# Performance work log

Hardware: AMD Instinct MI355X
Metric: run time of the kernel (lower is better)

The kernel has to match this reference:

```python
import jax, jax.numpy as jnp
import numpy as np

B, C, H, W = 2, 64, 512, 896


def setup_inputs() -> dict:
    key = jax.random.key(0)
    k1, k2 = jax.random.split(key)
    feature = jax.random.normal(k1, (B, C, H, W), dtype=jnp.float32)
    # flow in pixel units; a few pixels of motion is typical for video frames
    flow = jax.random.normal(k2, (B, 2, H, W), dtype=jnp.float32) * 3.0
    return {"feature": feature, "flow": flow}


def reference(feature, flow):
    # Flownet2-style Resample2d: out[b,c,y,x] = bilinear(feature[b,c], y+v, x+u)
    # with zero contribution from out-of-bounds taps.
    Bv, Cv, Hv, Wv = feature.shape
    HW = Hv * Wv
    gx = flow[:, 0] + jnp.arange(Wv, dtype=flow.dtype)[None, None, :]  # [B,H,W]
    gy = flow[:, 1] + jnp.arange(Hv, dtype=flow.dtype)[None, :, None]  # [B,H,W]
    x0f = jnp.floor(gx)
    y0f = jnp.floor(gy)
    wx = gx - x0f  # frac weights
    wy = gy - y0f
    x0 = x0f.astype(jnp.int32)
    y0 = y0f.astype(jnp.int32)
    feat = feature.reshape(Bv, Cv, HW)

    def corner(xi, yi, w):
        # zero out-of-bounds taps; clip indices so the gather is always legal
        valid = (xi >= 0) & (xi < Wv) & (yi >= 0) & (yi < Hv)
        idx = jnp.clip(yi, 0, Hv - 1) * Wv + jnp.clip(xi, 0, Wv - 1)  # [B,H,W]
        idx = jnp.broadcast_to(idx.reshape(Bv, 1, HW), (Bv, Cv, HW))
        v = jnp.take_along_axis(feat, idx, axis=2)  # [B,C,HW]
        wm = (w * valid.astype(w.dtype)).reshape(Bv, 1, HW)
        return v * wm

    out = (
        corner(x0, y0, (1.0 - wx) * (1.0 - wy))
        + corner(x0 + 1, y0, wx * (1.0 - wy))
        + corner(x0, y0 + 1, (1.0 - wx) * wy)
        + corner(x0 + 1, y0 + 1, wx * wy)
    )
    return out.reshape(Bv, Cv, Hv, Wv)
```

## Files before the change

kernel.cpp:

```cpp
#include <hip/hip_runtime.h>


#define Bv 2
#define Cv 64
#define Hv 512
#define Wv 896
#define HWsz (Hv * Wv)

#define TILE 64
#define CPB 2
#define NCG (Cv / CPB)
#define SW 91
#define SH 88
#define XOFF 12
#define YOFF 11
#define NSITES (SH * SW)
#define NTX (Wv / TILE)
#define NTY (Hv / TILE)
#define NTILES (NTX * NTY)
#define NBLK (Bv * NCG * NTILES)
#define THREADS 1024
#define NW (THREADS / 64)
#define KITERS (TILE * TILE / THREADS)

__global__ __launch_bounds__(THREADS, 8) void resample2d_kernel(
    const float* __restrict__ feature,
    const float* __restrict__ flow,
    float* __restrict__ out) {
    __shared__ float2 smem[NSITES];

    const int orig = blockIdx.x;
    const int wid = (orig & 7) * (NBLK / 8) + (orig >> 3);
    const int txi = wid % NTX;
    const int t2 = wid / NTX;
    const int tyi = t2 % NTY;
    const int zb = t2 / NTY;
    const int b = zb / NCG;
    const int c0 = (zb % NCG) * CPB;

    const int tx0 = txi * TILE;
    const int ty0 = tyi * TILE;
    const int xs = tx0 - XOFF;
    const int ys = ty0 - YOFF;

    const int tid = threadIdx.x;
    const int lane = tid & 63;
    const int wv = tid >> 6;

    const float* __restrict__ fbase = feature + ((size_t)b * Cv + c0) * HWsz;
    const float* __restrict__ flb = flow + (size_t)b * 2 * HWsz;
    float* __restrict__ ob = out + ((size_t)b * Cv + c0) * HWsz;

    const int px = tx0 + lane;
    float u[KITERS], v[KITERS];
#pragma unroll
    for (int k = 0; k < KITERS; ++k) {
        const int y = ty0 + wv + NW * k;
        const int pix = y * Wv + px;
        u[k] = flb[pix];
        v[k] = flb[HWsz + pix];
    }

    const bool interior = (xs >= 0) & (xs + SW <= Wv) & (ys >= 0) & (ys + SH <= Hv);
    if (interior) {
#pragma unroll
        for (int k = 0; k < 8; ++k) {
            const int p = tid + THREADS * k;
            if (p < NSITES) {
                const int r = p / SW;
                const int xx = p - r * SW;
                const float* src = fbase + (size_t)(ys + r) * Wv + (xs + xx);
                float2 val;
                val.x = src[0];
                val.y = src[HWsz];
                smem[p] = val;
            }
        }
    } else {
#pragma unroll
        for (int k = 0; k < 8; ++k) {
            const int p = tid + THREADS * k;
            if (p < NSITES) {
                const int r = p / SW;
                const int xx = p - r * SW;
                const int gy = ys + r;
                const int gx = xs + xx;
                float2 val = make_float2(0.0f, 0.0f);
                if (((unsigned)gy < (unsigned)Hv) & ((unsigned)gx < (unsigned)Wv)) {
                    const float* src = fbase + (size_t)gy * Wv + gx;
                    val.x = src[0];
                    val.y = src[HWsz];
                }
                smem[p] = val;
            }
        }
    }

    float wx[KITERS], wy[KITERS];
    int ac[KITERS];
    unsigned iw = 0;
#pragma unroll
    for (int k = 0; k < KITERS; ++k) {
        const int y = ty0 + wv + NW * k;
        const float gx = u[k] + (float)px;
        const float gy = v[k] + (float)y;
        const float x0f = floorf(gx);
        const float y0f = floorf(gy);
        wx[k] = gx - x0f;
        wy[k] = gy - y0f;
        const int lx = (int)x0f - xs;
        const int ly = (int)y0f - ys;
        const bool inwin = ((unsigned)lx <= (unsigned)(SW - 2)) &
                           ((unsigned)ly <= (unsigned)(SH - 2));
        iw |= inwin ? (1u << k) : 0u;
        const int lxc = min(max(lx, 0), SW - 2);
        const int lyc = min(max(ly, 0), SH - 2);
        ac[k] = lyc * SW + lxc;
    }

    __syncthreads();

#define READ(T, K)                        \
    do {                                  \
        const int a_ = ac[K];             \
        T[0] = smem[a_];                  \
        T[1] = smem[a_ + 1];              \
        T[2] = smem[a_ + SW];             \
        T[3] = smem[a_ + SW + 1];         \
    } while (0)

#define CONSUME(T, K)                                                          \
    do {                                                                       \
        if (!(iw & (1u << (K)))) {            \
            const int y_ = ty0 + wv + NW * (K);                                \
            const float gx_ = u[K] + (float)px;                                \
            const float gy_ = v[K] + (float)y_;                                \
            const int x0_ = (int)floorf(gx_);                                  \
            const int y0_ = (int)floorf(gy_);                                  \
            const int x1_ = x0_ + 1, y1_ = y0_ + 1;                            \
            const bool vx0 = (unsigned)x0_ < (unsigned)Wv;                     \
            const bool vx1 = (unsigned)x1_ < (unsigned)Wv;                     \
            const bool vy0 = (unsigned)y0_ < (unsigned)Hv;                     \
            const bool vy1 = (unsigned)y1_ < (unsigned)Hv;                     \
            const int cx0 = min(max(x0_, 0), Wv - 1);                          \
            const int cx1 = min(max(x1_, 0), Wv - 1);                          \
            const int cy0 = min(max(y0_, 0), Hv - 1);                          \
            const int cy1 = min(max(y1_, 0), Hv - 1);                          \
            _Pragma("unroll") for (int c = 0; c < CPB; ++c) {                  \
                const float* f = fbase + (size_t)c * HWsz;                     \
                ((float*)&T[0])[c] = (vx0 & vy0) ? f[cy0 * Wv + cx0] : 0.0f;   \
                ((float*)&T[1])[c] = (vx1 & vy0) ? f[cy0 * Wv + cx1] : 0.0f;   \
                ((float*)&T[2])[c] = (vx0 & vy1) ? f[cy1 * Wv + cx0] : 0.0f;   \
                ((float*)&T[3])[c] = (vx1 & vy1) ? f[cy1 * Wv + cx1] : 0.0f;   \
            }                                                                  \
        }                                                                      \
        const float omx = 1.0f - wx[K];                                        \
        const float omy = 1.0f - wy[K];                                        \
        const float w00 = omx * omy;                                           \
        const float w10 = wx[K] * omy;                                         \
        const float w01 = omx * wy[K];                                         \
        const float w11 = wx[K] * wy[K];                                       \
        const int pix_ = (ty0 + wv + NW * (K)) * Wv + px;                      \
        const float r0 = T[0].x * w00 + T[1].x * w10 +                         \
                         T[2].x * w01 + T[3].x * w11;                          \
        const float r1 = T[0].y * w00 + T[1].y * w10 +                         \
                         T[2].y * w01 + T[3].y * w11;                          \
        __builtin_nontemporal_store(r0, &ob[pix_]);                            \
        __builtin_nontemporal_store(r1, &ob[HWsz + pix_]);                     \
    } while (0)

    float2 tA[4], tB[4];
    READ(tA, 0);
    READ(tB, 1);
    CONSUME(tA, 0);
    READ(tA, 2);
    CONSUME(tB, 1);
    READ(tB, 3);
    CONSUME(tA, 2);
    CONSUME(tB, 3);

#undef READ
#undef CONSUME
}

extern "C" void kernel_launch(void* const* d_in, const int* in_sizes, int n_in,
                              void* d_out, int out_size, void* d_ws, size_t ws_size,
                              hipStream_t stream) {
    const float* feature = (const float*)d_in[0];
    const float* flow = (const float*)d_in[1];
    float* out = (float*)d_out;

    dim3 block(THREADS, 1, 1);
    dim3 grid(NBLK, 1, 1);
    resample2d_kernel<<<grid, block, 0, stream>>>(feature, flow, out);
}
```

Baseline: 428.2 us.

## Process four channel pairs per block with double-buffered LDS staging

Each block now handles four channel-pair groups instead of one. Flow, bilinear weights and window addresses are computed once and reused across the groups, and the next group's feature window is loaded into registers while the current group is computed from a double-buffered LDS tile. The aim is to amortise the flow load and per-pixel address math, and to overlap global loads with compute. In exchange LDS use doubles, the launch-bounds occupancy hint drops, grid size shrinks fourfold, and there are more barriers per block.

Result: no change. 425.3 us (-0.7%).

```diff
diff --git a/kernel.cpp b/kernel.cpp
--- a/kernel.cpp
+++ b/kernel.cpp
@@ -9,7 +9,9 @@
 
 #define TILE 64
 #define CPB 2
+#define GPB 4
 #define NCG (Cv / CPB)
+#define NCGB (NCG / GPB)
 #define SW 91
 #define SH 88
 #define XOFF 12
@@ -18,16 +20,20 @@
 #define NTX (Wv / TILE)
 #define NTY (Hv / TILE)
 #define NTILES (NTX * NTY)
-#define NBLK (Bv * NCG * NTILES)
+#define NBLK (Bv * NCGB * NTILES)
 #define THREADS 1024
 #define NW (THREADS / 64)
 #define KITERS (TILE * TILE / THREADS)
-
-__global__ __launch_bounds__(THREADS, 8) void resample2d_kernel(
+#define SITE_ITERS ((NSITES + THREADS - 1) / THREADS)
+#define LDS_BYTES (2 * NSITES * (int)sizeof(float2))
+
+__global__ __launch_bounds__(THREADS, 4) void resample2d_kernel(
     const float* __restrict__ feature,
     const float* __restrict__ flow,
     float* __restrict__ out) {
-    __shared__ float2 smem[NSITES];
+    extern __shared__ float2 smem[];
+    float2* const buf0 = smem;
+    float2* const buf1 = smem + NSITES;
 
     const int orig = blockIdx.x;
     const int wid = (orig & 7) * (NBLK / 8) + (orig >> 3);
@@ -35,8 +41,8 @@
     const int t2 = wid / NTX;
     const int tyi = t2 % NTY;
     const int zb = t2 / NTY;
-    const int b = zb / NCG;
-    const int c0 = (zb % NCG) * CPB;
+    const int b = zb / NCGB;
+    const int c0 = (zb % NCGB) * (GPB * CPB);
 
     const int tx0 = txi * TILE;
     const int ty0 = tyi * TILE;
@@ -53,50 +59,53 @@
 
     const int px = tx0 + lane;
     float u[KITERS], v[KITERS];
+    int pixk[KITERS];
 #pragma unroll
     for (int k = 0; k < KITERS; ++k) {
         const int y = ty0 + wv + NW * k;
-        const int pix = y * Wv + px;
-        u[k] = flb[pix];
-        v[k] = flb[HWsz + pix];
-    }
-
-    const bool interior = (xs >= 0) & (xs + SW <= Wv) & (ys >= 0) & (ys + SH <= Hv);
-    if (interior) {
+        pixk[k] = y * Wv + px;
+        u[k] = flb[pixk[k]];
+        v[k] = flb[HWsz + pixk[k]];
+    }
+
+    int sOff[SITE_ITERS];
+    int gOff[SITE_ITERS];
+    float vmask[SITE_ITERS];
 #pragma unroll
-        for (int k = 0; k < 8; ++k) {
-            const int p = tid + THREADS * k;
-            if (p < NSITES) {
-                const int r = p / SW;
-                const int xx = p - r * SW;
-                const float* src = fbase + (size_t)(ys + r) * Wv + (xs + xx);
-                float2 val;
-                val.x = src[0];
-                val.y = src[HWsz];
-                smem[p] = val;
-            }
-        }
-    } else {
-#pragma unroll
-        for (int k = 0; k < 8; ++k) {
-            const int p = tid + THREADS * k;
-            if (p < NSITES) {
-                const int r = p / SW;
-                const int xx = p - r * SW;
-                const int gy = ys + r;
-                const int gx = xs + xx;
-                float2 val = make_float2(0.0f, 0.0f);
-                if (((unsigned)gy < (unsigned)Hv) & ((unsigned)gx < (unsigned)Wv)) {
-                    const float* src = fbase + (size_t)gy * Wv + gx;
-                    val.x = src[0];
-                    val.y = src[HWsz];
-                }
-                smem[p] = val;
-            }
-        }
-    }
-
-    float wx[KITERS], wy[KITERS];
+    for (int i = 0; i < SITE_ITERS; ++i) {
+        const int p = tid + THREADS * i;
+        const int pc = (p < NSITES) ? p : (NSITES - 1);
+        const int r = pc / SW;
+        const int xx = pc - r * SW;
+        const int gy = ys + r;
+        const int gx = xs + xx;
+        const bool vd = ((unsigned)gy < (unsigned)Hv) & ((unsigned)gx < (unsigned)Wv);
+        gOff[i] = vd ? (gy * Wv + gx) : 0;
+        vmask[i] = vd ? 1.0f : 0.0f;
+        sOff[i] = pc;
+    }
+
+#define STAGE_LOAD(G)                                            \
+    do {                                                         \
+        const float* __restrict__ fg_ =                          \
+            fbase + (size_t)(G) * CPB * HWsz;                    \
+        _Pragma("unroll") for (int i = 0; i < SITE_ITERS; ++i) { \
+            a0[i] = fg_[gOff[i]];                                \
+            a1[i] = fg_[gOff[i] + HWsz];                         \
+        }                                                        \
+    } while (0)
+
+#define STAGE_WRITE(BUF)                                                   \
+    do {                                                                   \
+        _Pragma("unroll") for (int i = 0; i < SITE_ITERS; ++i) {           \
+            BUF[sOff[i]] = make_float2(a0[i] * vmask[i], a1[i] * vmask[i]); \
+        }                                                                  \
+    } while (0)
+
+    float a0[SITE_ITERS], a1[SITE_ITERS];
+    STAGE_LOAD(0);
+
+    float w00k[KITERS], w10k[KITERS], w01k[KITERS], w11k[KITERS];
     int ac[KITERS];
     unsigned iw = 0;
 #pragma unroll
@@ -106,8 +115,14 @@
         const float gy = v[k] + (float)y;
         const float x0f = floorf(gx);
         const float y0f = floorf(gy);
-        wx[k] = gx - x0f;
-        wy[k] = gy - y0f;
+        const float wx = gx - x0f;
+        const float wy = gy - y0f;
+        const float omx = 1.0f - wx;
+        const float omy = 1.0f - wy;
+        w00k[k] = omx * omy;
+        w10k[k] = wx * omy;
+        w01k[k] = omx * wy;
+        w11k[k] = wx * wy;
         const int lx = (int)x0f - xs;
         const int ly = (int)y0f - ys;
         const bool inwin = ((unsigned)lx <= (unsigned)(SW - 2)) &
@@ -118,69 +133,70 @@
         ac[k] = lyc * SW + lxc;
     }
 
-    __syncthreads();
-
-#define READ(T, K)                        \
-    do {                                  \
-        const int a_ = ac[K];             \
-        T[0] = smem[a_];                  \
-        T[1] = smem[a_ + 1];              \
-        T[2] = smem[a_ + SW];             \
-        T[3] = smem[a_ + SW + 1];         \
+#define COMPUTE(G, BUF)                                                        \
+    do {                                                                       \
+        float* __restrict__ og_ = ob + (size_t)(G) * CPB * HWsz;               \
+        const float* __restrict__ fg_ = fbase + (size_t)(G) * CPB * HWsz;      \
+        _Pragma("unroll") for (int k = 0; k < KITERS; ++k) {                   \
+            float2 t00 = BUF[ac[k]];                                           \
+            float2 t10 = BUF[ac[k] + 1];                                       \
+            float2 t01 = BUF[ac[k] + SW];                                      \
+            float2 t11 = BUF[ac[k] + SW + 1];                                  \
+            if (!(iw & (1u << k))) {          \
+                const int y_ = ty0 + wv + NW * k;                              \
+                const float gx_ = u[k] + (float)px;                            \
+                const float gy_ = v[k] + (float)y_;                            \
+                const int x0_ = (int)floorf(gx_);                              \
+                const int y0_ = (int)floorf(gy_);                              \
+                const int x1_ = x0_ + 1, y1_ = y0_ + 1;                        \
+                const bool vx0 = (unsigned)x0_ < (unsigned)Wv;                 \
+                const bool vx1 = (unsigned)x1_ < (unsigned)Wv;                 \
+                const bool vy0 = (unsigned)y0_ < (unsigned)Hv;                 \
+                const bool vy1 = (unsigned)y1_ < (unsigned)Hv;                 \
+                const int cx0 = min(max(x0_, 0), Wv - 1);                      \
+                const int cx1 = min(max(x1_, 0), Wv - 1);                      \
+                const int cy0 = min(max(y0_, 0), Hv - 1);                      \
+                const int cy1 = min(max(y1_, 0), Hv - 1);                      \
+                _Pragma("unroll") for (int c = 0; c < CPB; ++c) {              \
+                    const float* f = fg_ + (size_t)c * HWsz;                   \
+                    ((float*)&t00)[c] = (vx0 & vy0) ? f[cy0 * Wv + cx0] : 0.f; \
+                    ((float*)&t10)[c] = (vx1 & vy0) ? f[cy0 * Wv + cx1] : 0.f; \
+                    ((float*)&t01)[c] = (vx0 & vy1) ? f[cy1 * Wv + cx0] : 0.f; \
+                    ((float*)&t11)[c] = (vx1 & vy1) ? f[cy1 * Wv + cx1] : 0.f; \
+                }                                                              \
+            }                                                                  \
+            const float r0 = t00.x * w00k[k] + t10.x * w10k[k] +               \
+                             t01.x * w01k[k] + t11.x * w11k[k];                \
+            const float r1 = t00.y * w00k[k] + t10.y * w10k[k] +               \
+                             t01.y * w01k[k] + t11.y * w11k[k];                \
+            __builtin_nontemporal_store(r0, &og_[pixk[k]]);                    \
+            __builtin_nontemporal_store(r1, &og_[HWsz + pixk[k]]);             \
+        }                                                                      \
     } while (0)
 
-#define CONSUME(T, K)                                                          \
-    do {                                                                       \
-        if (!(iw & (1u << (K)))) {            \
-            const int y_ = ty0 + wv + NW * (K);                                \
-            const float gx_ = u[K] + (float)px;                                \
-            const float gy_ = v[K] + (float)y_;                                \
-            const int x0_ = (int)floorf(gx_);                                  \
-            const int y0_ = (int)floorf(gy_);                                  \
-            const int x1_ = x0_ + 1, y1_ = y0_ + 1;                            \
-            const bool vx0 = (unsigned)x0_ < (unsigned)Wv;                     \
-            const bool vx1 = (unsigned)x1_ < (unsigned)Wv;                     \
-            const bool vy0 = (unsigned)y0_ < (unsigned)Hv;                     \
-            const bool vy1 = (unsigned)y1_ < (unsigned)Hv;                     \
-            const int cx0 = min(max(x0_, 0), Wv - 1);                          \
-            const int cx1 = min(max(x1_, 0), Wv - 1);                          \
-            const int cy0 = min(max(y0_, 0), Hv - 1);                          \
-            const int cy1 = min(max(y1_, 0), Hv - 1);                          \
-            _Pragma("unroll") for (int c = 0; c < CPB; ++c) {                  \
-                const float* f = fbase + (size_t)c * HWsz;                     \
-                ((float*)&T[0])[c] = (vx0 & vy0) ? f[cy0 * Wv + cx0] : 0.0f;   \
-                ((float*)&T[1])[c] = (vx1 & vy0) ? f[cy0 * Wv + cx1] : 0.0f;   \
-                ((float*)&T[2])[c] = (vx0 & vy1) ? f[cy1 * Wv + cx0] : 0.0f;   \
-                ((float*)&T[3])[c] = (vx1 & vy1) ? f[cy1 * Wv + cx1] : 0.0f;   \
-            }                                                                  \
-        }                                                                      \
-        const float omx = 1.0f - wx[K];                                        \
-        const float omy = 1.0f - wy[K];                                        \
-        const float w00 = omx * omy;                                           \
-        const float w10 = wx[K] * omy;                                         \
-        const float w01 = omx * wy[K];                                         \
-        const float w11 = wx[K] * wy[K];                                       \
-        const int pix_ = (ty0 + wv + NW * (K)) * Wv + px;                      \
-        const float r0 = T[0].x * w00 + T[1].x * w10 +                         \
-                         T[2].x * w01 + T[3].x * w11;                          \
-        const float r1 = T[0].y * w00 + T[1].y * w10 +                         \
-                         T[2].y * w01 + T[3].y * w11;                          \
-        __builtin_nontemporal_store(r0, &ob[pix_]);                            \
-        __builtin_nontemporal_store(r1, &ob[HWsz + pix_]);                     \
-    } while (0)
-
-    float2 tA[4], tB[4];
-    READ(tA, 0);
-    READ(tB, 1);
-    CONSUME(tA, 0);
-    READ(tA, 2);
-    CONSUME(tB, 1);
-    READ(tB, 3);
-    CONSUME(tA, 2);
-    CONSUME(tB, 3);
-
-#undef READ
-#undef CONSUME
+    STAGE_WRITE(buf0);
+    __syncthreads();
+
+    STAGE_LOAD(1);
+    COMPUTE(0, buf0);
+    STAGE_WRITE(buf1);
+    __syncthreads();
+
+    STAGE_LOAD(2);
+    COMPUTE(1, buf1);
+    STAGE_WRITE(buf0);
+    __syncthreads();
+
+    STAGE_LOAD(3);
+    COMPUTE(2, buf0);
+    STAGE_WRITE(buf1);
+    __syncthreads();
+
+    COMPUTE(3, buf1);
+
+#undef STAGE_LOAD
+#undef STAGE_WRITE
+#undef COMPUTE
 }
 
 extern "C" void kernel_launch(void* const* d_in, const int* in_sizes, int n_in,
@@ -190,7 +206,14 @@
     const float* flow = (const float*)d_in[1];
     float* out = (float*)d_out;
 
+    static bool inited = false;
+    if (!inited) {
+        hipFuncSetAttribute((const void*)resample2d_kernel,
+                            hipFuncAttributeMaxDynamicSharedMemorySize, LDS_BYTES);
+        inited = true;
+    }
+
     dim3 block(THREADS, 1, 1);
     dim3 grid(NBLK, 1, 1);
-    resample2d_kernel<<<grid, block, 0, stream>>>(feature, flow, out);
+    resample2d_kernel<<<grid, block, LDS_BYTES, stream>>>(feature, flow, out);
 }
```
